# Kernel optimization log

Hardware: AMD Instinct MI355X
Metric: run time of the kernel (lower is better)

## Reference

```python
import jax, jax.numpy as jnp
import numpy as np

RC = 5.0  # cosine cutoff radius

def ssp(z):
    # shifted softplus, SchNet activation
    return jax.nn.softplus(z) - jnp.log(2.0).astype(z.dtype)

def setup_inputs():
    key = jax.random.key(0)
    ks = jax.random.split(key, 16)
    B, Na, Nn, G, F = 2, 2048, 48, 50, 128
    e = jax.random.normal(ks[0], (B, Na, 1), jnp.float32)
    x = jax.random.normal(ks[1], (B, Na, F), jnp.float32)
    t = jax.random.normal(ks[2], (B, Na, 1), jnp.float32)
    r_ij = jax.random.uniform(ks[3], (B, Na, Nn), jnp.float32) * 6.0  # some beyond cutoff
    neighbors = jax.random.randint(ks[4], (B, Na, Nn), 0, Na)
    pairwise_mask = jax.random.randint(ks[5], (B, Na, Nn), 0, 2).astype(jnp.int32)
    f_ij = jax.random.normal(ks[6], (B, Na, Nn, G), jnp.float32)
    def lin(k, fan_in, fan_out):
        return jax.random.normal(k, (fan_in, fan_out), jnp.float32) / np.sqrt(fan_in).astype(np.float32)
    Wf1 = lin(ks[7], G, F); bf1 = jnp.zeros((F,), jnp.float32)
    Wf2 = lin(ks[8], F, F); bf2 = jnp.zeros((F,), jnp.float32)
    Wq = lin(ks[9], F, F)
    Wk = lin(ks[10], F, F)
    Wv = lin(ks[11], F, F)
    Wo = lin(ks[12], F, F); bo = jnp.zeros((F,), jnp.float32)
    return dict(e=e, x=x, t=t, r_ij=r_ij, neighbors=neighbors, pairwise_mask=pairwise_mask,
                f_ij=f_ij, Wf1=Wf1, bf1=bf1, Wf2=Wf2, bf2=bf2, Wq=Wq, Wk=Wk, Wv=Wv, Wo=Wo, bo=bo)

def reference(e, x, t, r_ij, neighbors, pairwise_mask, f_ij,
              Wf1, bf1, Wf2, bf2, Wq, Wk, Wv, Wo, bo):
    B, Na, Nn = neighbors.shape
    F = x.shape[-1]
    # continuous filter from expanded distances: W = filter_network(2*f_ij - 1)
    W = 2.0 * f_ij - 1.0
    W = ssp(W @ Wf1 + bf1) @ Wf2 + bf2                # [B,Na,Nn,F]
    # cosine cutoff
    C = (0.5 * (jnp.cos(jnp.pi * r_ij / RC) + 1.0) * (r_ij < RC))[..., None]  # [B,Na,Nn,1]
    W = W * C
    # gather neighbor embeddings: y[b,i,n,:] = x[b, neighbors[b,i,n], :]
    idx = neighbors.reshape(B, Na * Nn)
    y = jnp.take_along_axis(x, idx[..., None], axis=1).reshape(B, Na, Nn, F)
    y_full = jnp.concatenate([x[:, :, None, :], y], axis=2)  # [B,Na,Nn+1,F] self + neighbors
    # cutoff-masked attention aggregation
    q = x @ Wq                                        # [B,Na,F]
    k = y_full @ Wk                                   # [B,Na,Nn+1,F]
    v = y_full @ Wv
    v = jnp.concatenate([v[:, :, :1, :], v[:, :, 1:, :] * W], axis=2)  # filter-modulated values
    scores = jnp.einsum('baf,banf->ban', q, k) / jnp.sqrt(jnp.float32(F))
    mask = jnp.concatenate([jnp.ones((B, Na, 1), bool), pairwise_mask.astype(bool)], axis=2)
    scores = jnp.where(mask, scores, jnp.float32(-1e9))
    attn = jax.nn.softmax(scores, axis=-1)
    m = jnp.einsum('ban,banf->baf', attn, v)
    m = ssp(m @ Wo + bo)                              # [B,Na,F]
    return (m, W)
```

## Files before the change

kernel.cpp:

```cpp
#include <hip/hip_runtime.h>

typedef unsigned int uint;
typedef unsigned short ushort;

#define B_  2
#define NA  2048
#define NN  48
#define G_  50
#define F_  128
#define NK  49
#define NROW (B_ * NA * NN)
#define NAT  (B_ * NA)

typedef short short8 __attribute__((ext_vector_type(8)));
typedef float floatx4 __attribute__((ext_vector_type(4)));

__device__ __forceinline__ float ssp(float z) {
  return fmaxf(z, 0.f) + __logf(1.f + __expf(-fabsf(z))) - 0.69314718055994531f;
}
__device__ __forceinline__ ushort f2bf(float x) {
  union { float f; uint u; } v; v.f = x;
  uint u = v.u;
  u += 0x7fffu + ((u >> 16) & 1u);
  return (ushort)(u >> 16);
}
__device__ __forceinline__ uint pk2bf(float x, float y) {
  return (uint)f2bf(x) | ((uint)f2bf(y) << 16);
}

extern "C" __global__ __launch_bounds__(256)
void prep_kernel(const float* __restrict__ Wf1, const float* __restrict__ Wf2,
                 const float* __restrict__ Wv, const float* __restrict__ Wo,
                 ushort* __restrict__ Wf1t, ushort* __restrict__ Wf2t,
                 ushort* __restrict__ Wvt, ushort* __restrict__ Wot)
{
  int gid = blockIdx.x * 256 + threadIdx.x;
  if (gid < 8192) {
    int n = gid >> 6, k = gid & 63;
    Wf1t[gid] = f2bf((k < G_) ? Wf1[(size_t)k * F_ + n] : 0.f);
  }
  for (int idx = gid; idx < 3 * 16384; idx += 24576) {
    int m = idx >> 14, e = idx & 16383;
    int n = e >> 7, k = e & 127;
    const float* src = (m == 0) ? Wf2 : (m == 1) ? Wv : Wo;
    ushort* dst = (m == 0) ? Wf2t : (m == 1) ? Wvt : Wot;
    dst[e] = f2bf(src[(size_t)k * F_ + n]);
  }
}

extern "C" __global__ __launch_bounds__(256, 4)
void qk_kernel(const float* __restrict__ x,
               const float* __restrict__ Wq, const float* __restrict__ Wk,
               float* __restrict__ Qo, float* __restrict__ Ko)
{
  __shared__ float xs[32 * 128];
  const int t = threadIdx.x;
  const int f = t & 127, h = t >> 7;
  const size_t Rb = (size_t)blockIdx.x * 32;
  const float* W = blockIdx.y ? Wk : Wq;
  float* O = blockIdx.y ? Ko : Qo;

  {
    const float4* src = (const float4*)(x + Rb * F_);
    float4* dst = (float4*)xs;
    #pragma unroll
    for (int k = 0; k < 4; ++k) dst[t + 256 * k] = src[t + 256 * k];
  }
  __syncthreads();

  float acc[16];
  #pragma unroll
  for (int j = 0; j < 16; ++j) acc[j] = 0.f;
  #pragma unroll
  for (int kc = 0; kc < 4; ++kc) {
    float wr[32];
    #pragma unroll
    for (int kk = 0; kk < 32; ++kk) wr[kk] = W[(size_t)(kc * 32 + kk) * F_ + f];
    #pragma unroll
    for (int j = 0; j < 16; ++j) {
      const float4* xr = (const float4*)&xs[(h * 16 + j) * 128 + kc * 32];
      #pragma unroll
      for (int qq = 0; qq < 8; ++qq) {
        float4 v = xr[qq];
        acc[j] += v.x * wr[qq * 4] + v.y * wr[qq * 4 + 1]
                + v.z * wr[qq * 4 + 2] + v.w * wr[qq * 4 + 3];
      }
    }
  }
  #pragma unroll
  for (int j = 0; j < 16; ++j)
    O[(Rb + h * 16 + j) * F_ + f] = acc[j];
}

extern "C" __global__ __launch_bounds__(256, 4)
void v_kernel(const float* __restrict__ x, const ushort* __restrict__ Wvt,
              float* __restrict__ Vo)
{
  __shared__ ushort xb[16 * 136];
  const int t = threadIdx.x;
  const int lane = t & 63, w = t >> 6;
  const int c16 = lane & 15, q = lane >> 4;
  const size_t Rb = (size_t)blockIdx.x * 16;

  {
    int row = t >> 4, col = (t & 15) * 8;
    float4 v0 = *(const float4*)(x + (Rb + row) * F_ + col);
    float4 v1 = *(const float4*)(x + (Rb + row) * F_ + col + 4);
    uint4 pk = { pk2bf(v0.x, v0.y), pk2bf(v0.z, v0.w),
                 pk2bf(v1.x, v1.y), pk2bf(v1.z, v1.w) };
    *(uint4*)((char*)xb + row * 272 + col * 2) = pk;
  }
  __syncthreads();

  short8 a[4];
  const char* ap = (const char*)xb + c16 * 272 + q * 16;
  #pragma unroll
  for (int s = 0; s < 4; ++s) a[s] = *(const short8*)(ap + s * 64);

  #pragma unroll
  for (int u = 0; u < 2; ++u) {
    int n = (w * 2 + u) * 16 + c16;
    const char* bb = (const char*)Wvt + n * 256 + q * 16;
    floatx4 acc = {0.f, 0.f, 0.f, 0.f};
    #pragma unroll
    for (int s = 0; s < 4; ++s) {
      short8 b = *(const short8*)(bb + s * 64);
      acc = __builtin_amdgcn_mfma_f32_16x16x32_bf16(a[s], b, acc, 0, 0, 0);
    }
    #pragma unroll
    for (int r = 0; r < 4; ++r)
      Vo[(Rb + q * 4 + r) * F_ + n] = acc[r];
  }
}

struct __align__(16) SmemF2 {
  union {
    ushort ft[128 * 72];
    ushort h1[128 * 136];
  } u;
  float C[128];
};

extern "C" __global__ __launch_bounds__(256, 4)
void filter_kernel(const float* __restrict__ fij, const float* __restrict__ r_ij,
                   const ushort* __restrict__ Wf1t, const float* __restrict__ bf1,
                   const ushort* __restrict__ Wf2t, const float* __restrict__ bf2p,
                   float* __restrict__ out_W)
{
  __shared__ SmemF2 sm;
  const int t = threadIdx.x;
  const int lane = t & 63, w = t >> 6;
  const int c16 = lane & 15, q = lane >> 4;
  const int m0 = w * 32;
  const size_t Rb = (size_t)blockIdx.x * 128;

  #pragma unroll
  for (int it = 0; it < 16; ++it) {
    int idx = t + it * 256;
    int row = idx >> 5, kp = idx & 31;
    uint pk = 0;
    if (kp < 25) {
      float2 v = *(const float2*)(fij + (Rb + row) * G_ + 2 * kp);
      pk = pk2bf(2.f * v.x - 1.f, 2.f * v.y - 1.f);
    }
    ((uint*)sm.u.ft)[row * 36 + kp] = pk;
  }
  if (t < 128) {
    float r = r_ij[Rb + t];
    sm.C[t] = (r < 5.0f) ? 0.5f * (cosf(0.62831853071795864769f * r) + 1.0f) : 0.0f;
  }
  __syncthreads();

  short8 a1[2][2];
  #pragma unroll
  for (int mt = 0; mt < 2; ++mt) {
    const char* ap = (const char*)sm.u.ft + (m0 + mt * 16 + c16) * 144 + q * 16;
    a1[mt][0] = *(const short8*)(ap);
    a1[mt][1] = *(const short8*)(ap + 64);
  }
  __syncthreads();

  short8 b1[8][2];
  #pragma unroll
  for (int nt = 0; nt < 8; ++nt) {
    const char* bb = (const char*)Wf1t + (nt * 16 + c16) * 128 + q * 16;
    b1[nt][0] = *(const short8*)(bb);
    b1[nt][1] = *(const short8*)(bb + 64);
  }

  #pragma unroll
  for (int nt = 0; nt < 8; ++nt) {
    int n = nt * 16 + c16;
    float bias = bf1[n];
    #pragma unroll
    for (int mt = 0; mt < 2; ++mt) {
      floatx4 acc = {0.f, 0.f, 0.f, 0.f};
      acc = __builtin_amdgcn_mfma_f32_16x16x32_bf16(a1[mt][0], b1[nt][0], acc, 0, 0, 0);
      acc = __builtin_amdgcn_mfma_f32_16x16x32_bf16(a1[mt][1], b1[nt][1], acc, 0, 0, 0);
      #pragma unroll
      for (int r = 0; r < 4; ++r) {
        int row = m0 + mt * 16 + q * 4 + r;
        sm.u.h1[row * 136 + n] = f2bf(ssp(acc[r] + bias));
      }
    }
  }

  short8 a2[2][4];
  #pragma unroll
  for (int mt = 0; mt < 2; ++mt) {
    const char* ap = (const char*)sm.u.h1 + (m0 + mt * 16 + c16) * 272 + q * 16;
    #pragma unroll
    for (int s = 0; s < 4; ++s) a2[mt][s] = *(const short8*)(ap + s * 64);
  }

  #pragma unroll
  for (int g = 0; g < 2; ++g) {
    short8 b2[4][4];
    #pragma unroll
    for (int j = 0; j < 4; ++j) {
      int n = (g * 4 + j) * 16 + c16;
      const char* bb = (const char*)Wf2t + n * 256 + q * 16;
      #pragma unroll
      for (int s = 0; s < 4; ++s) b2[j][s] = *(const short8*)(bb + s * 64);
    }
    #pragma unroll
    for (int j = 0; j < 4; ++j) {
      int n = (g * 4 + j) * 16 + c16;
      float bias = bf2p[n];
      #pragma unroll
      for (int mt = 0; mt < 2; ++mt) {
        floatx4 acc = {0.f, 0.f, 0.f, 0.f};
        #pragma unroll
        for (int s = 0; s < 4; ++s)
          acc = __builtin_amdgcn_mfma_f32_16x16x32_bf16(a2[mt][s], b2[j][s], acc, 0, 0, 0);
        #pragma unroll
        for (int r = 0; r < 4; ++r) {
          int row = m0 + mt * 16 + q * 4 + r;
          out_W[(Rb + row) * F_ + n] = (acc[r] + bias) * sm.C[row];
        }
      }
    }
  }
}

extern "C" __global__ __launch_bounds__(256, 4)
void attn_kernel(const float* __restrict__ Q, const float* __restrict__ K,
                 const float* __restrict__ V, const float* __restrict__ Wg,
                 const int* __restrict__ nbr, const int* __restrict__ pmask,
                 float* __restrict__ m_pre)
{
  const int t = threadIdx.x;
  const int lane = t & 63, w = t >> 6;
  const int a = blockIdx.x * 4 + w;
  const int b = a >> 11, i = a & 2047;
  const size_t base_nn = (size_t)a * NN;

  int nbrv = (lane < NN) ? nbr[base_nn + lane] : 0;
  int pmv  = (lane < NN) ? pmask[base_nn + lane] : 1;

  float2 q2 = *(const float2*)(Q + (size_t)a * F_ + lane * 2);

  float s_lane = -1e30f;
  #pragma unroll
  for (int n = 0; n < NK; ++n) {
    int src = (n == 0) ? i : __shfl(nbrv, (n > 0) ? n - 1 : 0);
    float2 k2 = *(const float2*)(K + ((size_t)b * NA + src) * F_ + lane * 2);
    float p = q2.x * k2.x + q2.y * k2.y;
    #pragma unroll
    for (int o = 32; o; o >>= 1) p += __shfl_xor(p, o);
    p *= 0.08838834764831845f;
    if (n > 0 && __shfl(pmv, n - 1) == 0) p = -1e9f;
    if (lane == n) s_lane = p;
  }

  float mx = s_lane;
  #pragma unroll
  for (int o = 32; o; o >>= 1) mx = fmaxf(mx, __shfl_xor(mx, o));
  float ev = (lane < NK) ? __expf(s_lane - mx) : 0.f;
  float sum = ev;
  #pragma unroll
  for (int o = 32; o; o >>= 1) sum += __shfl_xor(sum, o);
  float attn_l = ev / sum;

  float2 acc = {0.f, 0.f};
  #pragma unroll 8
  for (int n = 0; n < NK; ++n) {
    float an = __shfl(attn_l, n);
    int src = (n == 0) ? i : __shfl(nbrv, (n > 0) ? n - 1 : 0);
    float2 v2 = *(const float2*)(V + ((size_t)b * NA + src) * F_ + lane * 2);
    float2 w2 = {1.f, 1.f};
    if (n > 0) w2 = *(const float2*)(Wg + (base_nn + n - 1) * F_ + lane * 2);
    acc.x += an * w2.x * v2.x;
    acc.y += an * w2.y * v2.y;
  }
  *(float2*)(m_pre + (size_t)a * F_ + lane * 2) = acc;
}

extern "C" __global__ __launch_bounds__(256, 4)
void out_kernel(const float* __restrict__ m_pre, const ushort* __restrict__ Wot,
                const float* __restrict__ bo, float* __restrict__ out_m)
{
  __shared__ ushort xb[16 * 136];
  const int t = threadIdx.x;
  const int lane = t & 63, w = t >> 6;
  const int c16 = lane & 15, q = lane >> 4;
  const size_t Rb = (size_t)blockIdx.x * 16;

  {
    int row = t >> 4, col = (t & 15) * 8;
    float4 v0 = *(const float4*)(m_pre + (Rb + row) * F_ + col);
    float4 v1 = *(const float4*)(m_pre + (Rb + row) * F_ + col + 4);
    uint4 pk = { pk2bf(v0.x, v0.y), pk2bf(v0.z, v0.w),
                 pk2bf(v1.x, v1.y), pk2bf(v1.z, v1.w) };
    *(uint4*)((char*)xb + row * 272 + col * 2) = pk;
  }
  __syncthreads();

  short8 a[4];
  const char* ap = (const char*)xb + c16 * 272 + q * 16;
  #pragma unroll
  for (int s = 0; s < 4; ++s) a[s] = *(const short8*)(ap + s * 64);

  #pragma unroll
  for (int u = 0; u < 2; ++u) {
    int n = (w * 2 + u) * 16 + c16;
    const char* bb = (const char*)Wot + n * 256 + q * 16;
    floatx4 acc = {0.f, 0.f, 0.f, 0.f};
    #pragma unroll
    for (int s = 0; s < 4; ++s) {
      short8 b = *(const short8*)(bb + s * 64);
      acc = __builtin_amdgcn_mfma_f32_16x16x32_bf16(a[s], b, acc, 0, 0, 0);
    }
    float bias = bo[n];
    #pragma unroll
    for (int r = 0; r < 4; ++r)
      out_m[(Rb + q * 4 + r) * F_ + n] = ssp(acc[r] + bias);
  }
}

extern "C" void kernel_launch(void* const* d_in, const int* in_sizes, int n_in,
                              void* d_out, int out_size, void* d_ws, size_t ws_size,
                              hipStream_t stream) {
  const float* x   = (const float*)d_in[1];
  const float* r   = (const float*)d_in[3];
  const int*  nbr  = (const int*)d_in[4];
  const int*  pmk  = (const int*)d_in[5];
  const float* fij = (const float*)d_in[6];
  const float* Wf1 = (const float*)d_in[7];
  const float* bf1 = (const float*)d_in[8];
  const float* Wf2 = (const float*)d_in[9];
  const float* bf2p= (const float*)d_in[10];
  const float* Wq  = (const float*)d_in[11];
  const float* Wk  = (const float*)d_in[12];
  const float* Wv  = (const float*)d_in[13];
  const float* Wo  = (const float*)d_in[14];
  const float* bo  = (const float*)d_in[15];
  float* out_m = (float*)d_out;
  float* out_W = out_m + (size_t)NAT * F_;

  float* Qs = (float*)d_ws;
  float* Ks = Qs + (size_t)NAT * F_;
  float* Vs = Ks + (size_t)NAT * F_;
  float* Ms = Vs + (size_t)NAT * F_;
  ushort* Wf1t = (ushort*)(Ms + (size_t)NAT * F_);
  ushort* Wf2t = Wf1t + 128 * 64;
  ushort* Wvt  = Wf2t + 128 * 128;
  ushort* Wot  = Wvt  + 128 * 128;

  hipLaunchKernelGGL(prep_kernel, dim3(96), dim3(256), 0, stream,
                     Wf1, Wf2, Wv, Wo, Wf1t, Wf2t, Wvt, Wot);
  hipLaunchKernelGGL(qk_kernel, dim3(NAT / 32, 2), dim3(256), 0, stream,
                     x, Wq, Wk, Qs, Ks);
  hipLaunchKernelGGL(v_kernel, dim3(NAT / 16), dim3(256), 0, stream,
                     x, Wvt, Vs);
  hipLaunchKernelGGL(filter_kernel, dim3(NROW / 128), dim3(256), 0, stream,
                     fij, r, Wf1t, bf1, Wf2t, bf2p, out_W);
  hipLaunchKernelGGL(attn_kernel, dim3(NAT / 4), dim3(256), 0, stream,
                     Qs, Ks, Vs, out_W, nbr, pmk, Ms);
  hipLaunchKernelGGL(out_kernel, dim3(NAT / 16), dim3(256), 0, stream,
                     Ms, Wot, bo, out_m);
}
```

Before: 272.2 us.

## Parallelize attention scores per lane and vectorize GEMM output stores

The attention kernel now assigns one neighbor per lane: each lane reads its own full K row against Q staged in shared memory. This replaces 49 serial wave-wide shuffle reductions with a single per-lane dot product, and attention weights and source indices go through shared memory instead of shuffles. The small V and output GEMMs swap the MFMA operand order so each lane holds four contiguous output columns, allowing 16-byte vector stores and a vector bias load. Per-lane K row reads are uncoalesced across lanes (each lane strides a different row), which may cost memory efficiency.

Result: no change. 273.2 us (+0.4%).

```diff
diff --git a/kernel.cpp b/kernel.cpp
--- a/kernel.cpp
+++ b/kernel.cpp
@@ -112,24 +112,22 @@
   }
   __syncthreads();
 
-  short8 a[4];
+  short8 bx[4];
   const char* ap = (const char*)xb + c16 * 272 + q * 16;
   #pragma unroll
-  for (int s = 0; s < 4; ++s) a[s] = *(const short8*)(ap + s * 64);
+  for (int s = 0; s < 4; ++s) bx[s] = *(const short8*)(ap + s * 64);
 
   #pragma unroll
   for (int u = 0; u < 2; ++u) {
-    int n = (w * 2 + u) * 16 + c16;
-    const char* bb = (const char*)Wvt + n * 256 + q * 16;
+    int ntile = w * 2 + u;
+    const char* bb = (const char*)Wvt + (ntile * 16 + c16) * 256 + q * 16;
     floatx4 acc = {0.f, 0.f, 0.f, 0.f};
     #pragma unroll
     for (int s = 0; s < 4; ++s) {
-      short8 b = *(const short8*)(bb + s * 64);
-      acc = __builtin_amdgcn_mfma_f32_16x16x32_bf16(a[s], b, acc, 0, 0, 0);
-    }
-    #pragma unroll
-    for (int r = 0; r < 4; ++r)
-      Vo[(Rb + q * 4 + r) * F_ + n] = acc[r];
+      short8 wf = *(const short8*)(bb + s * 64);
+      acc = __builtin_amdgcn_mfma_f32_16x16x32_bf16(wf, bx[s], acc, 0, 0, 0);
+    }
+    *(floatx4*)(Vo + (Rb + c16) * F_ + ntile * 16 + q * 4) = acc;
   }
 }
 
@@ -249,45 +247,55 @@
                  const int* __restrict__ nbr, const int* __restrict__ pmask,
                  float* __restrict__ m_pre)
 {
+  __shared__ float qs[4][128];
+  __shared__ float attn_s[4][64];
+  __shared__ int   src_s[4][64];
   const int t = threadIdx.x;
   const int lane = t & 63, w = t >> 6;
   const int a = blockIdx.x * 4 + w;
   const int b = a >> 11, i = a & 2047;
   const size_t base_nn = (size_t)a * NN;
 
-  int nbrv = (lane < NN) ? nbr[base_nn + lane] : 0;
-  int pmv  = (lane < NN) ? pmask[base_nn + lane] : 1;
-
-  float2 q2 = *(const float2*)(Q + (size_t)a * F_ + lane * 2);
-
-  float s_lane = -1e30f;
-  #pragma unroll
-  for (int n = 0; n < NK; ++n) {
-    int src = (n == 0) ? i : __shfl(nbrv, (n > 0) ? n - 1 : 0);
-    float2 k2 = *(const float2*)(K + ((size_t)b * NA + src) * F_ + lane * 2);
-    float p = q2.x * k2.x + q2.y * k2.y;
-    #pragma unroll
-    for (int o = 32; o; o >>= 1) p += __shfl_xor(p, o);
-    p *= 0.08838834764831845f;
-    if (n > 0 && __shfl(pmv, n - 1) == 0) p = -1e9f;
-    if (lane == n) s_lane = p;
-  }
-
-  float mx = s_lane;
+  {
+    float2 q2 = *(const float2*)(Q + (size_t)a * F_ + lane * 2);
+    *(float2*)&qs[w][lane * 2] = q2;
+  }
+
+  int src = i;
+  int pm = 1;
+  if (lane >= 1 && lane <= NN) {
+    src = nbr[base_nn + lane - 1];
+    pm  = pmask[base_nn + lane - 1];
+  }
+  src_s[w][lane] = src;
+
+  float s = 0.f;
+  const float* Krow = K + ((size_t)b * NA + src) * F_;
+  #pragma unroll 8
+  for (int c = 0; c < 32; ++c) {
+    float4 k4 = *(const float4*)(Krow + c * 4);
+    float4 q4 = *(const float4*)&qs[w][c * 4];
+    s += q4.x * k4.x + q4.y * k4.y + q4.z * k4.z + q4.w * k4.w;
+  }
+  s *= 0.08838834764831845f;
+  if (lane >= 1 && pm == 0) s = -1e9f;
+  if (lane >= NK) s = -1e30f;
+
+  float mx = s;
   #pragma unroll
   for (int o = 32; o; o >>= 1) mx = fmaxf(mx, __shfl_xor(mx, o));
-  float ev = (lane < NK) ? __expf(s_lane - mx) : 0.f;
+  float ev = (lane < NK) ? __expf(s - mx) : 0.f;
   float sum = ev;
   #pragma unroll
   for (int o = 32; o; o >>= 1) sum += __shfl_xor(sum, o);
-  float attn_l = ev / sum;
+  attn_s[w][lane] = ev / sum;
 
   float2 acc = {0.f, 0.f};
   #pragma unroll 8
   for (int n = 0; n < NK; ++n) {
-    float an = __shfl(attn_l, n);
-    int src = (n == 0) ? i : __shfl(nbrv, (n > 0) ? n - 1 : 0);
-    float2 v2 = *(const float2*)(V + ((size_t)b * NA + src) * F_ + lane * 2);
+    float an = attn_s[w][n];
+    int   sr = src_s[w][n];
+    float2 v2 = *(const float2*)(V + ((size_t)b * NA + sr) * F_ + lane * 2);
     float2 w2 = {1.f, 1.f};
     if (n > 0) w2 = *(const float2*)(Wg + (base_nn + n - 1) * F_ + lane * 2);
     acc.x += an * w2.x * v2.x;
@@ -316,25 +324,29 @@
   }
   __syncthreads();
 
-  short8 a[4];
+  short8 bx[4];
   const char* ap = (const char*)xb + c16 * 272 + q * 16;
   #pragma unroll
-  for (int s = 0; s < 4; ++s) a[s] = *(const short8*)(ap + s * 64);
+  for (int s = 0; s < 4; ++s) bx[s] = *(const short8*)(ap + s * 64);
 
   #pragma unroll
   for (int u = 0; u < 2; ++u) {
-    int n = (w * 2 + u) * 16 + c16;
-    const char* bb = (const char*)Wot + n * 256 + q * 16;
+    int ntile = w * 2 + u;
+    const char* bb = (const char*)Wot + (ntile * 16 + c16) * 256 + q * 16;
     floatx4 acc = {0.f, 0.f, 0.f, 0.f};
     #pragma unroll
     for (int s = 0; s < 4; ++s) {
-      short8 b = *(const short8*)(bb + s * 64);
-      acc = __builtin_amdgcn_mfma_f32_16x16x32_bf16(a[s], b, acc, 0, 0, 0);
-    }
-    float bias = bo[n];
-    #pragma unroll
-    for (int r = 0; r < 4; ++r)
-      out_m[(Rb + q * 4 + r) * F_ + n] = ssp(acc[r] + bias);
+      short8 wf = *(const short8*)(bb + s * 64);
+      acc = __builtin_amdgcn_mfma_f32_16x16x32_bf16(wf, bx[s], acc, 0, 0, 0);
+    }
+    int n0 = ntile * 16 + q * 4;
+    float4 bv = *(const float4*)&bo[n0];
+    floatx4 outv;
+    outv[0] = ssp(acc[0] + bv.x);
+    outv[1] = ssp(acc[1] + bv.y);
+    outv[2] = ssp(acc[2] + bv.z);
+    outv[3] = ssp(acc[3] + bv.w);
+    *(floatx4*)(out_m + (Rb + c16) * F_ + n0) = outv;
   }
 }
 
```
